# Kernel tuning notes

Hardware: AMD Instinct MI355X
Metric: run time of the kernel (lower is better)

The kernel has to match this reference:

```python
import jax, jax.numpy as jnp
import numpy as np

B, L, D = 2, 2048, 512
E = 2
DI = E * D          # d_inner = 1024
DS = 16             # d_state
DC = 4              # d_conv
DR = D // 16        # dt_rank = 32
EPS = 1e-6


def setup_inputs() -> dict:
    key = jax.random.key(0)
    ks = jax.random.split(key, 12)
    s = 0.02
    # S4D-real init for A_log, as in mamba_ssm
    A_log = jnp.log(jnp.tile(jnp.arange(1, DS + 1, dtype=jnp.float32), (DI, 1)))
    return {
        "x": jax.random.normal(ks[0], (B, L, D), dtype=jnp.float32),
        "W_in": jax.random.normal(ks[1], (2 * DI, D), dtype=jnp.float32) * s,
        "conv_w": jax.random.normal(ks[2], (DI, 1, DC), dtype=jnp.float32) * 0.2,
        "conv_b": jnp.zeros((DI,), dtype=jnp.float32),
        "W_xproj": jax.random.normal(ks[3], (DR + 2 * DS, DI), dtype=jnp.float32) * s,
        "W_dt": jax.random.normal(ks[4], (DI, DR), dtype=jnp.float32) * s,
        "b_dt": jax.random.normal(ks[5], (DI,), dtype=jnp.float32) * 0.1,
        "A_log": A_log,
        "D_param": jnp.ones((DI,), dtype=jnp.float32),
        "W_out": jax.random.normal(ks[6], (D, DI), dtype=jnp.float32) * s,
        "ln_w": jnp.ones((D,), dtype=jnp.float32),
        "ln_b": jnp.zeros((D,), dtype=jnp.float32),
    }


def _mamba_layer(x, W_in, conv_w, conv_b, W_xproj, W_dt, b_dt, A_log, D_param, W_out, ln_w, ln_b):
    # in_proj (no bias): [B,L,D] -> [B,L,2*DI]
    xz = jnp.einsum('bld,ed->ble', x, W_in)
    xi, z = jnp.split(xz, 2, axis=-1)

    # depthwise causal conv1d over time + SiLU
    xt = jnp.transpose(xi, (0, 2, 1))                      # [B,DI,L]
    xt = jnp.pad(xt, ((0, 0), (0, 0), (DC - 1, 0)))        # causal left pad
    xc = jax.lax.conv_general_dilated(
        xt, conv_w, window_strides=(1,), padding='VALID',
        dimension_numbers=('NCH', 'OIH', 'NCH'), feature_group_count=DI)
    xc = jax.nn.silu(xc + conv_b[None, :, None])
    u = jnp.transpose(xc, (0, 2, 1))                       # [B,L,DI]

    # x_proj -> (dt, B, C)
    x_dbl = jnp.einsum('bld,ed->ble', u, W_xproj)          # [B,L,DR+2*DS]
    dt, Bm, Cm = jnp.split(x_dbl, [DR, DR + DS], axis=-1)
    delta = jax.nn.softplus(jnp.einsum('blr,dr->bld', dt, W_dt) + b_dt)  # [B,L,DI]

    A = -jnp.exp(A_log)                                    # [DI,DS]
    dA = jnp.exp(delta[..., None] * A)                     # [B,L,DI,DS]
    dBu = delta[..., None] * Bm[:, :, None, :] * u[..., None]

    def step(h, inputs):
        dA_t, dBu_t, C_t = inputs                          # [B,DI,DS],[B,DI,DS],[B,DS]
        h = dA_t * h + dBu_t
        y = jnp.einsum('bds,bs->bd', h, C_t)
        return h, y

    h0 = jnp.zeros((x.shape[0], DI, DS), dtype=x.dtype)
    _, ys = jax.lax.scan(step, h0, (jnp.moveaxis(dA, 1, 0),
                                    jnp.moveaxis(dBu, 1, 0),
                                    jnp.moveaxis(Cm, 1, 0)))
    y = jnp.moveaxis(ys, 0, 1) + u * D_param               # [B,L,DI]
    y = y * jax.nn.silu(z)
    out_m = jnp.einsum('ble,de->bld', y, W_out)            # [B,L,D]

    # LayerNorm(eps=1e-6) then residual add
    mu = out_m.mean(-1, keepdims=True)
    var = ((out_m - mu) ** 2).mean(-1, keepdims=True)
    normed = (out_m - mu) * jax.lax.rsqrt(var + EPS) * ln_w + ln_b
    return x + normed


def reference(x, W_in, conv_w, conv_b, W_xproj, W_dt, b_dt, A_log, D_param, W_out, ln_w, ln_b):
    return _mamba_layer(x, W_in, conv_w, conv_b, W_xproj, W_dt, b_dt,
                        A_log, D_param, W_out, ln_w, ln_b)
```

## Files before the change

kernel.cpp:

```cpp
#include <hip/hip_runtime.h>
#include <math.h>

#define B_  2
#define L_  2048
#define D_  512
#define DI_ 1024
#define DS_ 16
#define DC_ 4
#define DR_ 32
#define NX_ 64
#define NC_ 64
#define CT_ 32
#define KS_ 8
#define MC_ 32

typedef unsigned short u16;
typedef u16   u16x8  __attribute__((ext_vector_type(8)));
typedef __bf16 bf16x8 __attribute__((ext_vector_type(8)));
typedef float  f32x4  __attribute__((ext_vector_type(4)));

__device__ __forceinline__ float sigmoidf_(float v) { return 1.f / (1.f + __expf(-v)); }

__device__ __forceinline__ u16 f2bf(float f) {
    union { float f; unsigned u; } c; c.f = f;
    unsigned u = c.u + 0x7FFFu + ((c.u >> 16) & 1u);
    return (u16)(u >> 16);
}
__device__ __forceinline__ float bf2f(u16 v) {
    union { unsigned u; float f; } c; c.u = ((unsigned)v) << 16; return c.f;
}

__global__ void cast_all(const float* __restrict__ s0, u16* __restrict__ o0, int n0,
                         const float* __restrict__ s1, u16* __restrict__ o1, int n1,
                         const float* __restrict__ s2, u16* __restrict__ o2, int n2,
                         const float* __restrict__ s3, u16* __restrict__ o3, int n3) {
    int i = blockIdx.x * 256 + threadIdx.x;
    const float* s; u16* o; int j = i;
    if (j < n0) { s = s0; o = o0; }
    else { j -= n0;
        if (j < n1) { s = s1; o = o1; }
        else { j -= n1;
            if (j < n2) { s = s2; o = o2; }
            else { j -= n2;
                if (j < n3) { s = s3; o = o3; }
                else return; } } }
    const float4* p = reinterpret_cast<const float4*>(s) + (size_t)j * 2;
    float4 v0 = p[0], v1 = p[1];
    u16x8 r;
    r[0] = f2bf(v0.x); r[1] = f2bf(v0.y); r[2] = f2bf(v0.z); r[3] = f2bf(v0.w);
    r[4] = f2bf(v1.x); r[5] = f2bf(v1.y); r[6] = f2bf(v1.z); r[7] = f2bf(v1.w);
    reinterpret_cast<u16x8*>(o)[j] = r;
}

template<int K, int N0, int N1>
__global__ __launch_bounds__(512, 1) void gemm_mfma_nt(
    const u16* __restrict__ Ab, const u16* __restrict__ Bb,
    u16* __restrict__ out0, u16* __restrict__ out1) {
    __shared__ u16 As[256 * 64];
    __shared__ u16 Bs[128 * 64];
    const int bm = blockIdx.y * 256, bn = blockIdx.x * 128;
    const int t = threadIdx.x;
    const int w = t >> 6, l = t & 63;
    const int wm = (w >> 1) * 64, wn = (w & 1) * 64;
    const int lr = l & 15;
    const int lk = (l >> 4) * 8;

    f32x4 acc[4][4] = {};

    for (int k0 = 0; k0 < K; k0 += 64) {
        #pragma unroll
        for (int i = 0; i < 4; i++) {
            int q  = i * 512 + t;
            int r  = q >> 3;
            int c0 = ((q ^ r) & 7) << 3;
            __builtin_amdgcn_global_load_lds(
                (const __attribute__((address_space(1))) void*)(Ab + (size_t)(bm + r) * K + k0 + c0),
                (__attribute__((address_space(3))) void*)(As + (i * 512 + w * 64) * 8),
                16, 0, 0);
        }
        #pragma unroll
        for (int i = 0; i < 2; i++) {
            int q  = i * 512 + t;
            int r  = q >> 3;
            int c0 = ((q ^ r) & 7) << 3;
            __builtin_amdgcn_global_load_lds(
                (const __attribute__((address_space(1))) void*)(Bb + (size_t)(bn + r) * K + k0 + c0),
                (__attribute__((address_space(3))) void*)(Bs + (i * 512 + w * 64) * 8),
                16, 0, 0);
        }
        __syncthreads();
        #pragma unroll
        for (int kk = 0; kk < 2; kk++) {
            bf16x8 a[4], b[4];
            #pragma unroll
            for (int m = 0; m < 4; m++) {
                int row  = wm + m * 16 + lr;
                int byte = (row * 128 + (kk * 32 + lk) * 2) ^ ((row & 7) << 4);
                a[m] = *reinterpret_cast<const bf16x8*>(reinterpret_cast<const char*>(As) + byte);
            }
            #pragma unroll
            for (int n = 0; n < 4; n++) {
                int row  = wn + n * 16 + lr;
                int byte = (row * 128 + (kk * 32 + lk) * 2) ^ ((row & 7) << 4);
                b[n] = *reinterpret_cast<const bf16x8*>(reinterpret_cast<const char*>(Bs) + byte);
            }
            #pragma unroll
            for (int m = 0; m < 4; m++)
                #pragma unroll
                for (int n = 0; n < 4; n++)
                    acc[m][n] = __builtin_amdgcn_mfma_f32_16x16x32_bf16(a[m], b[n], acc[m][n], 0, 0, 0);
        }
        __syncthreads();
    }

    u16* obase = (bn < N0) ? out0 : out1;
    const int stride = (bn < N0) ? N0 : N1;
    const int bcol   = (bn < N0) ? bn : bn - N0;
    #pragma unroll
    for (int m = 0; m < 4; m++) {
        #pragma unroll
        for (int j = 0; j < 4; j++) {
            int row = bm + wm + m * 16 + (l >> 4) * 4 + j;
            #pragma unroll
            for (int n = 0; n < 4; n++)
                obase[(size_t)row * stride + bcol + wn + n * 16 + lr] = f2bf(acc[m][n][j]);
        }
    }
}

__global__ __launch_bounds__(256, 2) void xproj_mfma(
    const u16* __restrict__ xib, const float* __restrict__ cw,
    const float* __restrict__ cb, const u16* __restrict__ Bb,
    float* __restrict__ part) {
    __shared__ u16 As[128 * 64];
    __shared__ u16 Bs[64 * 64];
    const int ks = blockIdx.x;
    const int bm = blockIdx.y * 128;
    const int t = threadIdx.x;
    const int w = t >> 6, l = t & 63;
    const int wm = (w >> 1) * 64, wn = (w & 1) * 32;
    const int lr = l & 15;
    const int lk = (l >> 4) * 8;
    const int c8 = t & 7;
    const int rb = t >> 3;

    f32x4 acc[4][2] = {};

    for (int it = 0; it < 2; it++) {
        int k0 = ks * 128 + it * 64;
        int d0 = k0 + c8 * 8;
        float4 cw4[8]; float cb8[8];
        #pragma unroll
        for (int e = 0; e < 8; e++) {
            cw4[e] = *reinterpret_cast<const float4*>(cw + (d0 + e) * 4);
            cb8[e] = cb[d0 + e];
        }
        #pragma unroll
        for (int i = 0; i < 4; i++) {
            int r = rb + 32 * i;
            int m = bm + r;
            int lq = m & (L_ - 1);
            u16x8 wnd[4];
            #pragma unroll
            for (int j = 0; j < 4; j++) {
                int lt = lq - 3 + j;
                if (lt >= 0) {
                    wnd[j] = *reinterpret_cast<const u16x8*>(xib + (size_t)(m - 3 + j) * DI_ + d0);
                } else {
                    #pragma unroll
                    for (int e = 0; e < 8; e++) wnd[j][e] = 0;
                }
            }
            u16x8 uo;
            #pragma unroll
            for (int e = 0; e < 8; e++) {
                float a2 = cb8[e];
                a2 = fmaf(bf2f(wnd[0][e]), cw4[e].x, a2);
                a2 = fmaf(bf2f(wnd[1][e]), cw4[e].y, a2);
                a2 = fmaf(bf2f(wnd[2][e]), cw4[e].z, a2);
                a2 = fmaf(bf2f(wnd[3][e]), cw4[e].w, a2);
                float v = a2 * sigmoidf_(a2);
                uo[e] = f2bf(v);
            }
            int byte = (r * 128 + c8 * 16) ^ ((r & 7) << 4);
            *reinterpret_cast<u16x8*>(reinterpret_cast<char*>(As) + byte) = uo;
        }
        #pragma unroll
        for (int i = 0; i < 2; i++) {
            int q  = i * 256 + t;
            int r  = q >> 3;
            int c0 = ((q ^ r) & 7) << 3;
            __builtin_amdgcn_global_load_lds(
                (const __attribute__((address_space(1))) void*)(Bb + (size_t)r * 1024 + k0 + c0),
                (__attribute__((address_space(3))) void*)(Bs + (i * 256 + w * 64) * 8),
                16, 0, 0);
        }
        __syncthreads();
        #pragma unroll
        for (int kk = 0; kk < 2; kk++) {
            bf16x8 a[4], b[2];
            #pragma unroll
            for (int m = 0; m < 4; m++) {
                int row  = wm + m * 16 + lr;
                int byte = (row * 128 + (kk * 32 + lk) * 2) ^ ((row & 7) << 4);
                a[m] = *reinterpret_cast<const bf16x8*>(reinterpret_cast<const char*>(As) + byte);
            }
            #pragma unroll
            for (int n = 0; n < 2; n++) {
                int row  = wn + n * 16 + lr;
                int byte = (row * 128 + (kk * 32 + lk) * 2) ^ ((row & 7) << 4);
                b[n] = *reinterpret_cast<const bf16x8*>(reinterpret_cast<const char*>(Bs) + byte);
            }
            #pragma unroll
            for (int m = 0; m < 4; m++)
                #pragma unroll
                for (int n = 0; n < 2; n++)
                    acc[m][n] = __builtin_amdgcn_mfma_f32_16x16x32_bf16(a[m], b[n], acc[m][n], 0, 0, 0);
        }
        __syncthreads();
    }

    float* obase = part + (size_t)ks * (4096 * 64);
    #pragma unroll
    for (int m = 0; m < 4; m++) {
        #pragma unroll
        for (int j = 0; j < 4; j++) {
            int row = bm + wm + m * 16 + (l >> 4) * 4 + j;
            #pragma unroll
            for (int n = 0; n < 2; n++)
                obase[(size_t)row * 64 + wn + n * 16 + lr] = acc[m][n][j];
        }
    }
}

__global__ __launch_bounds__(256, 2) void oproj_mfma(
    const u16* __restrict__ Ab, const u16* __restrict__ Bb, u16* __restrict__ outb) {
    __shared__ u16 As[128 * 64];
    __shared__ u16 Bs[64 * 64];
    const int bn = blockIdx.x * 64;
    const int bm = blockIdx.y * 128;
    const int t = threadIdx.x;
    const int w = t >> 6, l = t & 63;
    const int wm = (w >> 1) * 64, wn = (w & 1) * 32;
    const int lr = l & 15;
    const int lk = (l >> 4) * 8;

    f32x4 acc[4][2] = {};

    for (int k0 = 0; k0 < 1024; k0 += 64) {
        #pragma unroll
        for (int i = 0; i < 4; i++) {
            int q  = i * 256 + t;
            int r  = q >> 3;
            int c0 = ((q ^ r) & 7) << 3;
            __builtin_amdgcn_global_load_lds(
                (const __attribute__((address_space(1))) void*)(Ab + (size_t)(bm + r) * 1024 + k0 + c0),
                (__attribute__((address_space(3))) void*)(As + (i * 256 + w * 64) * 8),
                16, 0, 0);
        }
        #pragma unroll
        for (int i = 0; i < 2; i++) {
            int q  = i * 256 + t;
            int r  = q >> 3;
            int c0 = ((q ^ r) & 7) << 3;
            __builtin_amdgcn_global_load_lds(
                (const __attribute__((address_space(1))) void*)(Bb + (size_t)(bn + r) * 1024 + k0 + c0),
                (__attribute__((address_space(3))) void*)(Bs + (i * 256 + w * 64) * 8),
                16, 0, 0);
        }
        __syncthreads();
        #pragma unroll
        for (int kk = 0; kk < 2; kk++) {
            bf16x8 a[4], b[2];
            #pragma unroll
            for (int m = 0; m < 4; m++) {
                int row  = wm + m * 16 + lr;
                int byte = (row * 128 + (kk * 32 + lk) * 2) ^ ((row & 7) << 4);
                a[m] = *reinterpret_cast<const bf16x8*>(reinterpret_cast<const char*>(As) + byte);
            }
            #pragma unroll
            for (int n = 0; n < 2; n++) {
                int row  = wn + n * 16 + lr;
                int byte = (row * 128 + (kk * 32 + lk) * 2) ^ ((row & 7) << 4);
                b[n] = *reinterpret_cast<const bf16x8*>(reinterpret_cast<const char*>(Bs) + byte);
            }
            #pragma unroll
            for (int m = 0; m < 4; m++)
                #pragma unroll
                for (int n = 0; n < 2; n++)
                    acc[m][n] = __builtin_amdgcn_mfma_f32_16x16x32_bf16(a[m], b[n], acc[m][n], 0, 0, 0);
        }
        __syncthreads();
    }

    #pragma unroll
    for (int m = 0; m < 4; m++) {
        #pragma unroll
        for (int j = 0; j < 4; j++) {
            int row = bm + wm + m * 16 + (l >> 4) * 4 + j;
            #pragma unroll
            for (int n = 0; n < 2; n++)
                outb[(size_t)row * D_ + bn + wn + n * 16 + lr] = f2bf(acc[m][n][j]);
        }
    }
}

__global__ __launch_bounds__(256) void reduce_dt(
    const float* __restrict__ part, const float* __restrict__ Wdt,
    const float* __restrict__ bdt, float* __restrict__ xdbl,
    u16* __restrict__ deltab) {
    __shared__ float Wl[256 * 33];
    __shared__ float dts[MC_][DR_];
    const int t  = threadIdx.x;
    const int d0 = blockIdx.x * 256;
    const int m0 = blockIdx.y * MC_;

    for (int i = t; i < MC_ * DR_; i += 256) {
        int m = i >> 5, r = i & 31;
        float s = 0.f;
        #pragma unroll
        for (int ks = 0; ks < KS_; ks++) s += part[(size_t)ks * (4096 * 64) + (m0 + m) * 64 + r];
        dts[m][r] = s;
    }
    if (blockIdx.x == 0) {
        for (int i = t; i < MC_ * 64; i += 256) {
            int m = i >> 6, n = i & 63;
            float s = 0.f;
            #pragma unroll
            for (int ks = 0; ks < KS_; ks++) s += part[(size_t)ks * (4096 * 64) + (m0 + m) * 64 + n];
            xdbl[(size_t)(m0 + m) * 64 + n] = s;
        }
    }
    {
        const float4* src = reinterpret_cast<const float4*>(Wdt + (size_t)d0 * DR_);
        #pragma unroll
        for (int i = 0; i < 8; i++) {
            int e = (i * 256 + t);
            int r4 = e & 7, row = e >> 3;
            float4 v = src[e];
            float* dst = &Wl[row * 33 + r4 * 4];
            dst[0] = v.x; dst[1] = v.y; dst[2] = v.z; dst[3] = v.w;
        }
    }
    __syncthreads();

    float wreg[DR_];
    #pragma unroll
    for (int r = 0; r < DR_; r++) wreg[r] = Wl[t * 33 + r];
    const float bias = bdt[d0 + t];

    for (int m = 0; m < MC_; m++) {
        float a0 = bias, a1 = 0.f, a2 = 0.f, a3 = 0.f;
        #pragma unroll
        for (int r = 0; r < DR_; r += 4) {
            a0 = fmaf(dts[m][r],     wreg[r],     a0);
            a1 = fmaf(dts[m][r + 1], wreg[r + 1], a1);
            a2 = fmaf(dts[m][r + 2], wreg[r + 2], a2);
            a3 = fmaf(dts[m][r + 3], wreg[r + 3], a3);
        }
        float acc = (a0 + a1) + (a2 + a3);
        float sp  = fmaxf(acc, 0.f) + __logf(1.f + __expf(-fabsf(acc)));
        deltab[(size_t)(m0 + m) * DI_ + d0 + t] = f2bf(sp);
    }
}

__global__ void scan_p1(const u16* __restrict__ xib, const float* __restrict__ cw,
                        const float* __restrict__ cb, const u16* __restrict__ deltab,
                        const float* __restrict__ xdbl, const float* __restrict__ A_log,
                        u16* __restrict__ hzb, u16* __restrict__ pAb) {
    const int d = blockIdx.x * 256 + threadIdx.x;
    const int c = blockIdx.y;
    const int b = blockIdx.z;
    __shared__ float Brow[CT_][DS_];
    for (int i = threadIdx.x; i < CT_ * DS_; i += 256) {
        int t = i >> 4, s = i & 15;
        Brow[t][s] = xdbl[(size_t)(b * L_ + c * CT_ + t) * NX_ + DR_ + s];
    }
    __syncthreads();
    float a[DS_], h[DS_], p[DS_];
    #pragma unroll
    for (int s = 0; s < DS_; s++) {
        a[s] = -__expf(A_log[d * DS_ + s]);
        h[s] = 0.f; p[s] = 1.f;
    }
    const float4 cwv = *reinterpret_cast<const float4*>(cw + d * 4);
    const float cbd = cb[d];
    size_t base = (size_t)(b * L_ + c * CT_) * DI_ + d;
    float w0 = 0.f, w1 = 0.f, w2 = 0.f;
    if (c > 0) {
        w0 = bf2f(xib[base - 3 * DI_]);
        w1 = bf2f(xib[base - 2 * DI_]);
        w2 = bf2f(xib[base - 1 * DI_]);
    }
    #pragma unroll 2
    for (int t = 0; t < CT_; t++) {
        float xt = bf2f(xib[base + (size_t)t * DI_]);
        float cv = fmaf(w0, cwv.x, fmaf(w1, cwv.y, fmaf(w2, cwv.z, fmaf(xt, cwv.w, cbd))));
        float uv = cv * sigmoidf_(cv);
        w0 = w1; w1 = w2; w2 = xt;
        float dl = bf2f(deltab[base + (size_t)t * DI_]);
        float dlu = dl * uv;
        #pragma unroll
        for (int s = 0; s < DS_; s++) {
            float dA = __expf(dl * a[s]);
            p[s] *= dA;
            h[s] = fmaf(dA, h[s], dlu * Brow[t][s]);
        }
    }
    size_t o = ((size_t)(b * NC_ + c) * DI_ + d) * DS_;
    u16x8 hv0, hv1, pv0, pv1;
    #pragma unroll
    for (int s = 0; s < 8; s++) {
        hv0[s] = f2bf(h[s]);     hv1[s] = f2bf(h[s + 8]);
        pv0[s] = f2bf(p[s]);     pv1[s] = f2bf(p[s + 8]);
    }
    *reinterpret_cast<u16x8*>(hzb + o)     = hv0;
    *reinterpret_cast<u16x8*>(hzb + o + 8) = hv1;
    *reinterpret_cast<u16x8*>(pAb + o)     = pv0;
    *reinterpret_cast<u16x8*>(pAb + o + 8) = pv1;
}

__global__ __launch_bounds__(256) void carry(const u16* __restrict__ hzb,
                                             const u16* __restrict__ pAb,
                                             u16* __restrict__ hinb) {
    __shared__ float Hs[NC_][128];
    __shared__ float Ps[NC_][128];
    const int t  = threadIdx.x;
    const int g0 = blockIdx.x * 128;
    for (int i = t; i < NC_ * 128; i += 256) {
        int c = i >> 7, j = i & 127;
        int g = g0 + j;
        int b = g >> 14, ds = g & (DI_ * DS_ - 1);
        size_t o = (size_t)(b * NC_ + c) * (DI_ * DS_) + ds;
        Hs[c][j] = bf2f(hzb[o]);
        Ps[c][j] = bf2f(pAb[o]);
    }
    __syncthreads();
    if (t < 128) {
        float h = 0.f;
        #pragma unroll 4
        for (int c = 0; c < NC_; c++) {
            float hzc = Hs[c][t], pac = Ps[c][t];
            Hs[c][t] = h;
            h = fmaf(pac, h, hzc);
        }
    }
    __syncthreads();
    for (int i = t; i < NC_ * 128; i += 256) {
        int c = i >> 7, j = i & 127;
        int g = g0 + j;
        int b = g >> 14, ds = g & (DI_ * DS_ - 1);
        size_t o = (size_t)(b * NC_ + c) * (DI_ * DS_) + ds;
        hinb[o] = f2bf(Hs[c][j]);
    }
}

__global__ void scan_p2(const u16* __restrict__ xib, const float* __restrict__ cw,
                        const float* __restrict__ cb, const u16* __restrict__ deltab,
                        const float* __restrict__ xdbl, const float* __restrict__ A_log,
                        const u16* __restrict__ hinb, const u16* __restrict__ zb,
                        const float* __restrict__ Dp, u16* __restrict__ yvb) {
    const int d = blockIdx.x * 256 + threadIdx.x;
    const int c = blockIdx.y;
    const int b = blockIdx.z;
    __shared__ float Brow[CT_][DS_];
    __shared__ float Crow[CT_][DS_];
    for (int i = threadIdx.x; i < CT_ * DS_; i += 256) {
        int t = i >> 4, s = i & 15;
        size_t rb = (size_t)(b * L_ + c * CT_ + t) * NX_;
        Brow[t][s] = xdbl[rb + DR_ + s];
        Crow[t][s] = xdbl[rb + DR_ + DS_ + s];
    }
    __syncthreads();
    float a[DS_], h[DS_];
    size_t ho = ((size_t)(b * NC_ + c) * DI_ + d) * DS_;
    #pragma unroll
    for (int s = 0; s < DS_; s++) {
        a[s] = -__expf(A_log[d * DS_ + s]);
        h[s] = bf2f(hinb[ho + s]);
    }
    const float4 cwv = *reinterpret_cast<const float4*>(cw + d * 4);
    const float cbd = cb[d];
    float Dpd = Dp[d];
    size_t base = (size_t)(b * L_ + c * CT_) * DI_ + d;
    float w0 = 0.f, w1 = 0.f, w2 = 0.f;
    if (c > 0) {
        w0 = bf2f(xib[base - 3 * DI_]);
        w1 = bf2f(xib[base - 2 * DI_]);
        w2 = bf2f(xib[base - 1 * DI_]);
    }
    #pragma unroll 2
    for (int t = 0; t < CT_; t++) {
        float xt = bf2f(xib[base + (size_t)t * DI_]);
        float cv = fmaf(w0, cwv.x, fmaf(w1, cwv.y, fmaf(w2, cwv.z, fmaf(xt, cwv.w, cbd))));
        float uv = cv * sigmoidf_(cv);
        w0 = w1; w1 = w2; w2 = xt;
        float dl = bf2f(deltab[base + (size_t)t * DI_]);
        float dlu = dl * uv;
        float acc = 0.f;
        #pragma unroll
        for (int s = 0; s < DS_; s++) {
            float dA = __expf(dl * a[s]);
            h[s] = fmaf(dA, h[s], dlu * Brow[t][s]);
            acc = fmaf(h[s], Crow[t][s], acc);
        }
        float zv = bf2f(zb[base + (size_t)t * DI_]);
        float yval = fmaf(uv, Dpd, acc);
        yvb[base + (size_t)t * DI_] = f2bf(yval * (zv * sigmoidf_(zv)));
    }
}

__global__ void ln_res(const u16* __restrict__ omb, const float* __restrict__ x,
                       const float* __restrict__ lw, const float* __restrict__ lb,
                       float* __restrict__ out) {
    const int row = blockIdx.x;
    const u16* r = omb + (size_t)row * D_;
    float v0 = bf2f(r[threadIdx.x]), v1 = bf2f(r[threadIdx.x + 256]);
    float s = v0 + v1, sq = v0 * v0 + v1 * v1;
    #pragma unroll
    for (int off = 32; off; off >>= 1) {
        s  += __shfl_down(s, off);
        sq += __shfl_down(sq, off);
    }
    __shared__ float ss[4], ssq[4];
    int w = threadIdx.x >> 6;
    if ((threadIdx.x & 63) == 0) { ss[w] = s; ssq[w] = sq; }
    __syncthreads();
    float ts  = ss[0] + ss[1] + ss[2] + ss[3];
    float tsq = ssq[0] + ssq[1] + ssq[2] + ssq[3];
    float mu  = ts * (1.f / 512.f);
    float var = tsq * (1.f / 512.f) - mu * mu;
    float inv = rsqrtf(var + 1e-6f);
    size_t i0 = (size_t)row * D_ + threadIdx.x;
    out[i0]       = x[i0]       + (v0 - mu) * inv * lw[threadIdx.x]       + lb[threadIdx.x];
    out[i0 + 256] = x[i0 + 256] + (v1 - mu) * inv * lw[threadIdx.x + 256] + lb[threadIdx.x + 256];
}

extern "C" void kernel_launch(void* const* d_in, const int* in_sizes, int n_in,
                              void* d_out, int out_size, void* d_ws, size_t ws_size,
                              hipStream_t stream) {
    const float* x      = (const float*)d_in[0];
    const float* W_in   = (const float*)d_in[1];
    const float* conv_w = (const float*)d_in[2];
    const float* conv_b = (const float*)d_in[3];
    const float* W_xp   = (const float*)d_in[4];
    const float* W_dt   = (const float*)d_in[5];
    const float* b_dt   = (const float*)d_in[6];
    const float* A_log  = (const float*)d_in[7];
    const float* Dp     = (const float*)d_in[8];
    const float* W_out  = (const float*)d_in[9];
    const float* ln_w   = (const float*)d_in[10];
    const float* ln_b   = (const float*)d_in[11];
    float* out = (float*)d_out;

    const size_t NBL = (size_t)B_ * L_ * DI_;
    u16* xib  = (u16*)d_ws;
    u16* zb   = xib + NBL;
    u16* yvb  = zb  + NBL;
    u16* omb  = yvb + NBL;
    u16* xb   = omb + (size_t)B_ * L_ * D_;
    u16* wb   = xb  + (size_t)B_ * L_ * D_;
    u16* wxb  = wb  + (size_t)2 * DI_ * D_;
    u16* wob  = wxb + (size_t)NX_ * DI_;
    u16* deltab = wob + (size_t)D_ * DI_;
    u16* hzb  = deltab + NBL;
    u16* pAb  = hzb + (size_t)B_ * NC_ * DI_ * DS_;
    u16* hinb = pAb + (size_t)B_ * NC_ * DI_ * DS_;
    float* xdbl  = (float*)(hinb + (size_t)B_ * NC_ * DI_ * DS_);
    float* part  = xdbl + (size_t)B_ * L_ * NX_;

    const int n0 = B_ * L_ * D_ / 8, n1 = 2 * DI_ * D_ / 8;
    const int n2 = NX_ * DI_ / 8,    n3 = D_ * DI_ / 8;
    cast_all<<<(n0 + n1 + n2 + n3 + 255) / 256, 256, 0, stream>>>(
        x, xb, n0, W_in, wb, n1, W_xp, wxb, n2, W_out, wob, n3);
    gemm_mfma_nt<512, 1024, 1024>
        <<<dim3(2048 / 128, 4096 / 256), 512, 0, stream>>>(xb, wb, xib, zb);
    xproj_mfma<<<dim3(KS_, 4096 / 128), 256, 0, stream>>>(xib, conv_w, conv_b, wxb, part);
    reduce_dt<<<dim3(DI_ / 256, (B_ * L_) / MC_), 256, 0, stream>>>(part, W_dt, b_dt, xdbl, deltab);
    scan_p1<<<dim3(DI_ / 256, NC_, B_), 256, 0, stream>>>(xib, conv_w, conv_b, deltab, xdbl, A_log, hzb, pAb);
    carry<<<(B_ * DI_ * DS_) / 128, 256, 0, stream>>>(hzb, pAb, hinb);
    scan_p2<<<dim3(DI_ / 256, NC_, B_), 256, 0, stream>>>(xib, conv_w, conv_b, deltab, xdbl, A_log, hinb, zb, Dp, yvb);
    oproj_mfma<<<dim3(D_ / 64, 4096 / 128), 256, 0, stream>>>(yvb, wob, omb);
    ln_res<<<B_ * L_, 256, 0, stream>>>(omb, x, ln_w, ln_b, out);
}
```

Before: 131.3 us.

## Shrink in_proj GEMM tile, swizzle block order, store xproj partials as bf16

The in_proj GEMM moves from 256x128 tiles with 512 threads to 128x128 tiles with 256 threads and two blocks per CU, which doubles the block count. The in_proj and out_proj GEMMs also remap block indices with an XCD-style swizzle so that neighbouring tiles land on the same die and share L2. The split-K partials from x_proj are now written as bf16 instead of fp32, halving that intermediate traffic. The cost is lower precision in the summed dt/B/C projections, plus less operand reuse per in_proj tile.

```diff
diff --git a/kernel.cpp b/kernel.cpp
--- a/kernel.cpp
+++ b/kernel.cpp
@@ -53,12 +53,15 @@
 }
 
 template<int K, int N0, int N1>
-__global__ __launch_bounds__(512, 1) void gemm_mfma_nt(
+__global__ __launch_bounds__(256, 2) void gemm_mfma_nt(
     const u16* __restrict__ Ab, const u16* __restrict__ Bb,
     u16* __restrict__ out0, u16* __restrict__ out1) {
-    __shared__ u16 As[256 * 64];
+    __shared__ u16 As[128 * 64];
     __shared__ u16 Bs[128 * 64];
-    const int bm = blockIdx.y * 256, bn = blockIdx.x * 128;
+    const int lin = blockIdx.y * gridDim.x + blockIdx.x;
+    const int q8  = (gridDim.x * gridDim.y) >> 3;
+    const int swz = (lin & 7) * q8 + (lin >> 3);
+    const int bm = (swz / gridDim.x) * 128, bn = (swz % gridDim.x) * 128;
     const int t = threadIdx.x;
     const int w = t >> 6, l = t & 63;
     const int wm = (w >> 1) * 64, wn = (w & 1) * 64;
@@ -70,22 +73,16 @@
     for (int k0 = 0; k0 < K; k0 += 64) {
         #pragma unroll
         for (int i = 0; i < 4; i++) {
-            int q  = i * 512 + t;
+            int q  = i * 256 + t;
             int r  = q >> 3;
             int c0 = ((q ^ r) & 7) << 3;
             __builtin_amdgcn_global_load_lds(
                 (const __attribute__((address_space(1))) void*)(Ab + (size_t)(bm + r) * K + k0 + c0),
-                (__attribute__((address_space(3))) void*)(As + (i * 512 + w * 64) * 8),
+                (__attribute__((address_space(3))) void*)(As + (i * 256 + w * 64) * 8),
                 16, 0, 0);
-        }
-        #pragma unroll
-        for (int i = 0; i < 2; i++) {
-            int q  = i * 512 + t;
-            int r  = q >> 3;
-            int c0 = ((q ^ r) & 7) << 3;
             __builtin_amdgcn_global_load_lds(
                 (const __attribute__((address_space(1))) void*)(Bb + (size_t)(bn + r) * K + k0 + c0),
-                (__attribute__((address_space(3))) void*)(Bs + (i * 512 + w * 64) * 8),
+                (__attribute__((address_space(3))) void*)(Bs + (i * 256 + w * 64) * 8),
                 16, 0, 0);
         }
         __syncthreads();
@@ -131,7 +128,7 @@
 __global__ __launch_bounds__(256, 2) void xproj_mfma(
     const u16* __restrict__ xib, const float* __restrict__ cw,
     const float* __restrict__ cb, const u16* __restrict__ Bb,
-    float* __restrict__ part) {
+    u16* __restrict__ part) {
     __shared__ u16 As[128 * 64];
     __shared__ u16 Bs[64 * 64];
     const int ks = blockIdx.x;
@@ -220,7 +217,7 @@
         __syncthreads();
     }
 
-    float* obase = part + (size_t)ks * (4096 * 64);
+    u16* obase = part + (size_t)ks * (4096 * 64);
     #pragma unroll
     for (int m = 0; m < 4; m++) {
         #pragma unroll
@@ -228,7 +225,7 @@
             int row = bm + wm + m * 16 + (l >> 4) * 4 + j;
             #pragma unroll
             for (int n = 0; n < 2; n++)
-                obase[(size_t)row * 64 + wn + n * 16 + lr] = acc[m][n][j];
+                obase[(size_t)row * 64 + wn + n * 16 + lr] = f2bf(acc[m][n][j]);
         }
     }
 }
@@ -237,8 +234,11 @@
     const u16* __restrict__ Ab, const u16* __restrict__ Bb, u16* __restrict__ outb) {
     __shared__ u16 As[128 * 64];
     __shared__ u16 Bs[64 * 64];
-    const int bn = blockIdx.x * 64;
-    const int bm = blockIdx.y * 128;
+    const int lin = blockIdx.y * gridDim.x + blockIdx.x;
+    const int q8  = (gridDim.x * gridDim.y) >> 3;
+    const int swz = (lin & 7) * q8 + (lin >> 3);
+    const int bn = (swz % gridDim.x) * 64;
+    const int bm = (swz / gridDim.x) * 128;
     const int t = threadIdx.x;
     const int w = t >> 6, l = t & 63;
     const int wm = (w >> 1) * 64, wn = (w & 1) * 32;
@@ -306,7 +306,7 @@
 }
 
 __global__ __launch_bounds__(256) void reduce_dt(
-    const float* __restrict__ part, const float* __restrict__ Wdt,
+    const u16* __restrict__ part, const float* __restrict__ Wdt,
     const float* __restrict__ bdt, float* __restrict__ xdbl,
     u16* __restrict__ deltab) {
     __shared__ float Wl[256 * 33];
@@ -319,7 +319,7 @@
         int m = i >> 5, r = i & 31;
         float s = 0.f;
         #pragma unroll
-        for (int ks = 0; ks < KS_; ks++) s += part[(size_t)ks * (4096 * 64) + (m0 + m) * 64 + r];
+        for (int ks = 0; ks < KS_; ks++) s += bf2f(part[(size_t)ks * (4096 * 64) + (m0 + m) * 64 + r]);
         dts[m][r] = s;
     }
     if (blockIdx.x == 0) {
@@ -327,7 +327,7 @@
             int m = i >> 6, n = i & 63;
             float s = 0.f;
             #pragma unroll
-            for (int ks = 0; ks < KS_; ks++) s += part[(size_t)ks * (4096 * 64) + (m0 + m) * 64 + n];
+            for (int ks = 0; ks < KS_; ks++) s += bf2f(part[(size_t)ks * (4096 * 64) + (m0 + m) * 64 + n]);
             xdbl[(size_t)(m0 + m) * 64 + n] = s;
         }
     }
@@ -566,15 +566,15 @@
     u16* hzb  = deltab + NBL;
     u16* pAb  = hzb + (size_t)B_ * NC_ * DI_ * DS_;
     u16* hinb = pAb + (size_t)B_ * NC_ * DI_ * DS_;
-    float* xdbl  = (float*)(hinb + (size_t)B_ * NC_ * DI_ * DS_);
-    float* part  = xdbl + (size_t)B_ * L_ * NX_;
+    u16* part = hinb + (size_t)B_ * NC_ * DI_ * DS_;
+    float* xdbl = (float*)(part + (size_t)KS_ * 4096 * 64);
 
     const int n0 = B_ * L_ * D_ / 8, n1 = 2 * DI_ * D_ / 8;
     const int n2 = NX_ * DI_ / 8,    n3 = D_ * DI_ / 8;
     cast_all<<<(n0 + n1 + n2 + n3 + 255) / 256, 256, 0, stream>>>(
         x, xb, n0, W_in, wb, n1, W_xp, wxb, n2, W_out, wob, n3);
     gemm_mfma_nt<512, 1024, 1024>
-        <<<dim3(2048 / 128, 4096 / 256), 512, 0, stream>>>(xb, wb, xib, zb);
+        <<<dim3(2048 / 128, 4096 / 128), 256, 0, stream>>>(xb, wb, xib, zb);
     xproj_mfma<<<dim3(KS_, 4096 / 128), 256, 0, stream>>>(xib, conv_w, conv_b, wxb, part);
     reduce_dt<<<dim3(DI_ / 256, (B_ * L_) / MC_), 256, 0, stream>>>(part, W_dt, b_dt, xdbl, deltab);
     scan_p1<<<dim3(DI_ / 256, NC_, B_), 256, 0, stream>>>(xib, conv_w, conv_b, deltab, xdbl, A_log, hzb, pAb);
```

Result: faster. 123.9 us (-5.6%).
